# Performance work log

Measured on AMD Instinct MI355X. Metric: run time of the kernel, lower is better.

## Reference

```python
import jax, jax.numpy as jnp
import numpy as np
import math

B, N, DIM = 4, 2048, 768
HEADS, DIM_HEAD = 12, 64
SCALE = math.sqrt(DIM_HEAD)


def setup_inputs() -> dict:
    key = jax.random.key(0)
    ks = jax.random.split(key, 5)
    inner = HEADS * DIM_HEAD
    x = jax.random.normal(ks[0], (B, N, DIM), dtype=jnp.float32)
    # Linear weights stored as [in, out] so y = x @ W (equivalent to torch Linear with W.T)
    w_q = jax.random.normal(ks[1], (DIM, inner), dtype=jnp.float32) * 0.02
    w_k = jax.random.normal(ks[2], (DIM, inner), dtype=jnp.float32) * 0.02
    w_v = jax.random.normal(ks[3], (DIM, inner), dtype=jnp.float32) * 0.02
    w_o = jax.random.normal(ks[4], (inner, DIM), dtype=jnp.float32) * 0.02
    b_o = jnp.zeros((DIM,), dtype=jnp.float32)
    return {"x": x, "w_q": w_q, "w_k": w_k, "w_v": w_v, "w_o": w_o, "b_o": b_o}


def _split_heads(t):
    # [b, n, h*d] -> [b, h, n, d]
    b, n, _ = t.shape
    return t.reshape(b, n, HEADS, DIM_HEAD).transpose(0, 2, 1, 3)


def reference(x, w_q, w_k, w_v, w_o, b_o):
    # context = x (self-attention, kv_include_self=False)
    q = _split_heads(x @ w_q)  # [b,h,n,d]
    k = _split_heads(x @ w_k)
    v = _split_heads(x @ w_v)
    scores = jnp.einsum("bhnd,bhmd->bhnm", q, k) / SCALE  # [b,h,n,n]
    attn = jax.nn.softmax(scores, axis=-1)  # dropout p=0 -> identity
    h = jnp.einsum("bhnm,bhmd->bhnd", attn, v)  # [b,h,n,d]
    H = h.transpose(0, 2, 1, 3).reshape(x.shape[0], x.shape[1], HEADS * DIM_HEAD)
    out = H @ w_o + b_o
    return out
```

## Files before the change

### kernel.cpp

```cpp
#include <hip/hip_runtime.h>
#include <hip/hip_bf16.h>
#include <cstdint>
#include <cstddef>

#define HEADS 12
#define DHEAD 64
#define SEQ   2048
#define DIMM  768
#define BATCH 4
#define MROWS (BATCH*SEQ)
#define BH    (BATCH*HEADS)
#define SCL_Q 0.18033688011112042f

typedef __attribute__((ext_vector_type(8))) short short8;
typedef __attribute__((ext_vector_type(4))) short short4v;
typedef __attribute__((ext_vector_type(4))) float floatx4;

__device__ __forceinline__ unsigned short f2bf(float f) {
    union { float f; uint32_t u; } v; v.f = f;
    uint32_t u = v.u;
    u += 0x7fffu + ((u >> 16) & 1u);
    return (unsigned short)(u >> 16);
}
__device__ __forceinline__ float bf2f(unsigned short h) {
    union { uint32_t u; float f; } v; v.u = ((uint32_t)h) << 16;
    return v.f;
}
#if __has_builtin(__builtin_amdgcn_perm)
__device__ __forceinline__ uint32_t pkbf(float a, float b) {
    union { float f; uint32_t u; } ua, ub; ua.f = a; ub.f = b;
    return __builtin_amdgcn_perm(ub.u + 0x8000u, ua.u + 0x8000u, 0x07060302u);
}
#else
__device__ __forceinline__ uint32_t pkbf(float a, float b) {
    __hip_bfloat162 h = __float22bfloat162_rn(make_float2(a, b));
    uint32_t u; __builtin_memcpy(&u, &h, 4); return u;
}
#endif
__device__ __forceinline__ float fexp2(float x) {
#if __has_builtin(__builtin_amdgcn_exp2f)
    return __builtin_amdgcn_exp2f(x);
#else
    return exp2f(x);
#endif
}

#if __has_builtin(__builtin_amdgcn_global_load_lds)
#define HAVE_GLDS 1
__device__ __forceinline__ void glds16(const unsigned short* g, unsigned short* l) {
    __builtin_amdgcn_global_load_lds(
        (const __attribute__((address_space(1))) unsigned int*)g,
        (__attribute__((address_space(3))) unsigned int*)l, 16, 0, 0);
}
#else
#define HAVE_GLDS 0
#endif

__device__ __forceinline__ int detect_f32(const uint32_t* xw, int tid) {
    __shared__ int cnt_;
    if (tid == 0) cnt_ = 0;
    __syncthreads();
    uint32_t w = xw[(size_t)(tid & 255) * 4096];
    float av = fabsf(bf2f((unsigned short)(w & 0xFFFFu)));
    atomicAdd(&cnt_, (av >= 9.0949e-13f && av <= 256.0f) ? 1 : 0);
    __syncthreads();
    return (cnt_ < 192) ? 1 : 0;
}

__global__ __launch_bounds__(256) void prep(
    const void* __restrict__ x,
    const void* __restrict__ wq, const void* __restrict__ wk,
    const void* __restrict__ wv, const void* __restrict__ wo,
    unsigned short* __restrict__ xc,
    unsigned short* __restrict__ wtq, unsigned short* __restrict__ wtk,
    unsigned short* __restrict__ wtv, unsigned short* __restrict__ wto)
{
    const int tid = threadIdx.x;
    const int isf32 = detect_f32((const uint32_t*)x, tid);
    const int blk = blockIdx.x;

    if (blk < 2304) {
        __shared__ unsigned short tile[32][33];
        const int m = blk / 576, rr = blk % 576;
        const void* src; unsigned short* dst;
        switch (m) {
            case 0: src = wq; dst = wtq; break;
            case 1: src = wk; dst = wtk; break;
            case 2: src = wv; dst = wtv; break;
            default: src = wo; dst = wto; break;
        }
        const float* srcf = (const float*)src;
        const unsigned short* srcs = (const unsigned short*)src;
        const int tx = tid & 31, ty = tid >> 5;
        const int k0 = (rr % 24) * 32;
        const int n0 = (rr / 24) * 32;
        #pragma unroll
        for (int it = 0; it < 4; it++) {
            int r = ty + it * 8;
            size_t idx = (size_t)(k0 + r) * DIMM + n0 + tx;
            tile[r][tx] = isf32 ? f2bf(srcf[idx]) : srcs[idx];
        }
        __syncthreads();
        #pragma unroll
        for (int it = 0; it < 4; it++) {
            int r = ty + it * 8;
            dst[(size_t)(n0 + r) * DIMM + k0 + tx] = tile[tx][r];
        }
    } else {
        const size_t i0 = ((size_t)(blk - 2304) * 256 + tid) * 8;
        if (isf32) {
            const float* xf = (const float*)x;
            float4 a = *(const float4*)&xf[i0];
            float4 b = *(const float4*)&xf[i0 + 4];
            short8 s = { (short)f2bf(a.x), (short)f2bf(a.y), (short)f2bf(a.z), (short)f2bf(a.w),
                         (short)f2bf(b.x), (short)f2bf(b.y), (short)f2bf(b.z), (short)f2bf(b.w) };
            *(short8*)&xc[i0] = s;
        } else {
            *(short8*)&xc[i0] = *(const short8*)&((const unsigned short*)x)[i0];
        }
    }
}

__global__ __launch_bounds__(256) void gemm_bt(
    const unsigned short* __restrict__ A,
    const unsigned short* __restrict__ Wt0,
    const unsigned short* __restrict__ Wt1,
    const unsigned short* __restrict__ Wt2,
    void* __restrict__ O0, void* __restrict__ O1, void* __restrict__ O2,
    const void* __restrict__ bias,
    const uint32_t* __restrict__ xsample,
    int mode_base)
{
    const int mode = mode_base + blockIdx.z;
    const unsigned short* Wt = (mode == 1) ? Wt1 : (mode == 2) ? Wt2 : Wt0;
    void* OutV               = (mode == 1) ? O1  : (mode == 2) ? O2  : O0;
    unsigned short* Out16 = (unsigned short*)OutV;
    float* Outf           = (float*)OutV;

    int isf32 = 0;
    if (mode == 3) isf32 = detect_f32(xsample, threadIdx.x);

    __shared__ unsigned short As[128 * 64];
    __shared__ unsigned short Bs[128 * 64];

    const int tid  = threadIdx.x;
    const int wid  = tid >> 6;
    const int lane = tid & 63;
    const int l16  = lane & 15;
    const int quad = lane >> 4;
    const int wm   = wid & 1;
    const int wn   = wid >> 1;
    const int bm   = blockIdx.x * 128;
    const int bn   = blockIdx.y * 128;
    const bool swap = (mode != 2);

    floatx4 acc[4][4];
    #pragma unroll
    for (int i = 0; i < 4; i++)
        #pragma unroll
        for (int j = 0; j < 4; j++)
            acc[i][j] = floatx4{0.f, 0.f, 0.f, 0.f};

    for (int kk = 0; kk < DIMM; kk += 64) {
        #pragma unroll
        for (int t = 0; t < 4; t++) {
            const int c  = t * 256 + tid;
            const int r  = c >> 3;
            const int lc = (((c & 7) ^ (r & 7))) * 8;
#if HAVE_GLDS
            glds16(&A [(size_t)(bm + r) * DIMM + kk + lc], &As[(t * 256 + wid * 64) * 8]);
            glds16(&Wt[(size_t)(bn + r) * DIMM + kk + lc], &Bs[(t * 256 + wid * 64) * 8]);
#else
            *(short8*)&As[c * 8] = *(const short8*)&A [(size_t)(bm + r) * DIMM + kk + lc];
            *(short8*)&Bs[c * 8] = *(const short8*)&Wt[(size_t)(bn + r) * DIMM + kk + lc];
#endif
        }
        __syncthreads();
        #pragma unroll
        for (int ks = 0; ks < 2; ks++) {
            const int ph = ((ks * 4 + quad) ^ (l16 & 7)) * 8;
            short8 xa[4], wb[4];
            #pragma unroll
            for (int t = 0; t < 4; t++)
                xa[t] = *(const short8*)&As[(wm * 64 + t * 16 + l16) * 64 + ph];
            #pragma unroll
            for (int t = 0; t < 4; t++)
                wb[t] = *(const short8*)&Bs[(wn * 64 + t * 16 + l16) * 64 + ph];
            if (swap) {
                #pragma unroll
                for (int mt = 0; mt < 4; mt++)
                    #pragma unroll
                    for (int nt = 0; nt < 4; nt++)
                        acc[mt][nt] = __builtin_amdgcn_mfma_f32_16x16x32_bf16(
                            wb[mt], xa[nt], acc[mt][nt], 0, 0, 0);
            } else {
                #pragma unroll
                for (int mt = 0; mt < 4; mt++)
                    #pragma unroll
                    for (int nt = 0; nt < 4; nt++)
                        acc[mt][nt] = __builtin_amdgcn_mfma_f32_16x16x32_bf16(
                            xa[mt], wb[nt], acc[mt][nt], 0, 0, 0);
            }
        }
        __syncthreads();
    }

    if (!swap) {
        #pragma unroll
        for (int nt = 0; nt < 4; nt++) {
            const int gcol = bn + wn * 64 + nt * 16 + l16;
            #pragma unroll
            for (int mt = 0; mt < 4; mt++) {
                const int grow0 = bm + wm * 64 + mt * 16 + quad * 4;
                const int b = grow0 >> 11, n0 = grow0 & 2047;
                const int h = gcol >> 6,  d  = gcol & 63;
                size_t addr = ((size_t)(b * HEADS + h) * DHEAD + d) * SEQ + n0;
                short4v pk = { (short)f2bf(acc[mt][nt][0]), (short)f2bf(acc[mt][nt][1]),
                               (short)f2bf(acc[mt][nt][2]), (short)f2bf(acc[mt][nt][3]) };
                *(short4v*)&Out16[addr] = pk;
            }
        }
    } else {
        #pragma unroll
        for (int nt = 0; nt < 4; nt++) {
            const int grow = bm + wm * 64 + nt * 16 + l16;
            #pragma unroll
            for (int mt = 0; mt < 4; mt++) {
                const int gcol0 = bn + wn * 64 + mt * 16 + quad * 4;
                float v0 = acc[mt][nt][0], v1 = acc[mt][nt][1];
                float v2 = acc[mt][nt][2], v3 = acc[mt][nt][3];
                if (mode == 0) { v0 *= SCL_Q; v1 *= SCL_Q; v2 *= SCL_Q; v3 *= SCL_Q; }
                if (mode == 3) {
                    if (isf32) {
                        float4 bv = *(const float4*)&((const float*)bias)[gcol0];
                        float4 o = { v0 + bv.x, v1 + bv.y, v2 + bv.z, v3 + bv.w };
                        *(float4*)&Outf[(size_t)grow * DIMM + gcol0] = o;
                    } else {
                        const unsigned short* bb = &((const unsigned short*)bias)[gcol0];
                        short4v pk = { (short)f2bf(v0 + bf2f(bb[0])),
                                       (short)f2bf(v1 + bf2f(bb[1])),
                                       (short)f2bf(v2 + bf2f(bb[2])),
                                       (short)f2bf(v3 + bf2f(bb[3])) };
                        *(short4v*)&Out16[(size_t)grow * DIMM + gcol0] = pk;
                    }
                } else {
                    const int b = grow >> 11, n = grow & 2047;
                    const int h = gcol0 >> 6, d = gcol0 & 63;
                    size_t addr = ((size_t)(b * HEADS + h) * SEQ + n) * DHEAD + d;
                    short4v pk = { (short)f2bf(v0), (short)f2bf(v1),
                                   (short)f2bf(v2), (short)f2bf(v3) };
                    *(short4v*)&Out16[addr] = pk;
                }
            }
        }
    }
}

__global__ __launch_bounds__(256) void gemm_o64(
    const unsigned short* __restrict__ A,
    const unsigned short* __restrict__ Wt,
    void* __restrict__ Out,
    const void* __restrict__ bias,
    const uint32_t* __restrict__ xsample)
{
    unsigned short* Out16 = (unsigned short*)Out;
    float* Outf           = (float*)Out;
    const int isf32 = detect_f32(xsample, threadIdx.x);

    __shared__ unsigned short As[128 * 64];
    __shared__ unsigned short Bs[64 * 64];

    const int tid  = threadIdx.x;
    const int wid  = tid >> 6;
    const int lane = tid & 63;
    const int l16  = lane & 15;
    const int quad = lane >> 4;
    const int wm   = wid & 1;
    const int wn   = wid >> 1;
    const int bm   = blockIdx.x * 128;
    const int bn   = blockIdx.y * 64;

    floatx4 acc[2][4];
    #pragma unroll
    for (int i = 0; i < 2; i++)
        #pragma unroll
        for (int j = 0; j < 4; j++)
            acc[i][j] = floatx4{0.f, 0.f, 0.f, 0.f};

    for (int kk = 0; kk < DIMM; kk += 64) {
        #pragma unroll
        for (int t = 0; t < 4; t++) {
            const int c  = t * 256 + tid;
            const int r  = c >> 3;
            const int lc = (((c & 7) ^ (r & 7))) * 8;
#if HAVE_GLDS
            glds16(&A[(size_t)(bm + r) * DIMM + kk + lc], &As[(t * 256 + wid * 64) * 8]);
#else
            *(short8*)&As[c * 8] = *(const short8*)&A[(size_t)(bm + r) * DIMM + kk + lc];
#endif
        }
        #pragma unroll
        for (int t = 0; t < 2; t++) {
            const int c  = t * 256 + tid;
            const int r  = c >> 3;
            const int lc = (((c & 7) ^ (r & 7))) * 8;
#if HAVE_GLDS
            glds16(&Wt[(size_t)(bn + r) * DIMM + kk + lc], &Bs[(t * 256 + wid * 64) * 8]);
#else
            *(short8*)&Bs[c * 8] = *(const short8*)&Wt[(size_t)(bn + r) * DIMM + kk + lc];
#endif
        }
        __syncthreads();
        #pragma unroll
        for (int ks = 0; ks < 2; ks++) {
            const int ph = ((ks * 4 + quad) ^ (l16 & 7)) * 8;
            short8 xa[4], wb[2];
            #pragma unroll
            for (int t = 0; t < 4; t++)
                xa[t] = *(const short8*)&As[(wm * 64 + t * 16 + l16) * 64 + ph];
            #pragma unroll
            for (int t = 0; t < 2; t++)
                wb[t] = *(const short8*)&Bs[(wn * 32 + t * 16 + l16) * 64 + ph];
            #pragma unroll
            for (int mt = 0; mt < 2; mt++)
                #pragma unroll
                for (int nt = 0; nt < 4; nt++)
                    acc[mt][nt] = __builtin_amdgcn_mfma_f32_16x16x32_bf16(
                        wb[mt], xa[nt], acc[mt][nt], 0, 0, 0);
        }
        __syncthreads();
    }

    #pragma unroll
    for (int nt = 0; nt < 4; nt++) {
        const int grow = bm + wm * 64 + nt * 16 + l16;
        #pragma unroll
        for (int mt = 0; mt < 2; mt++) {
            const int gcol0 = bn + wn * 32 + mt * 16 + quad * 4;
            const float v0 = acc[mt][nt][0], v1 = acc[mt][nt][1];
            const float v2 = acc[mt][nt][2], v3 = acc[mt][nt][3];
            if (isf32) {
                float4 bv = *(const float4*)&((const float*)bias)[gcol0];
                float4 o = { v0 + bv.x, v1 + bv.y, v2 + bv.z, v3 + bv.w };
                *(float4*)&Outf[(size_t)grow * DIMM + gcol0] = o;
            } else {
                const unsigned short* bb = &((const unsigned short*)bias)[gcol0];
                short4v pk = { (short)f2bf(v0 + bf2f(bb[0])),
                               (short)f2bf(v1 + bf2f(bb[1])),
                               (short)f2bf(v2 + bf2f(bb[2])),
                               (short)f2bf(v3 + bf2f(bb[3])) };
                *(short4v*)&Out16[(size_t)grow * DIMM + gcol0] = pk;
            }
        }
    }
}

__global__ __launch_bounds__(256, 3) void attn(
    const unsigned short* __restrict__ Q,
    const unsigned short* __restrict__ K,
    const unsigned short* __restrict__ Vt,
    unsigned short* __restrict__ Hout)
{
    __shared__ unsigned short KsB[2 * 64 * 64];
    __shared__ unsigned short VsB[2 * 64 * 64];
    __shared__ unsigned short Ps[8][16 * 64];

    const int tid  = threadIdx.x;
    const int wid  = tid >> 6;
    const int lane = tid & 63;
    const int l16  = lane & 15;
    const int quad = lane >> 4;
    const int sw   = l16 & 7;

    const int bh = blockIdx.x % BH;
    const int qt = blockIdx.x / BH;

    short8 qf[2][2];
    #pragma unroll
    for (int t = 0; t < 2; t++) {
        const int qrow = qt * 128 + wid * 32 + t * 16 + l16;
        const size_t qbase = ((size_t)bh * SEQ + qrow) * DHEAD;
        qf[t][0] = *(const short8*)&Q[qbase + quad * 8];
        qf[t][1] = *(const short8*)&Q[qbase + 32 + quad * 8];
    }

    const short8 ones = { (short)0x3F80, (short)0x3F80, (short)0x3F80, (short)0x3F80,
                          (short)0x3F80, (short)0x3F80, (short)0x3F80, (short)0x3F80 };

    floatx4 ot[2][4];
    floatx4 acc_l[2];
    #pragma unroll
    for (int t = 0; t < 2; t++) {
        acc_l[t] = floatx4{0.f, 0.f, 0.f, 0.f};
        #pragma unroll
        for (int i = 0; i < 4; i++) ot[t][i] = floatx4{0.f, 0.f, 0.f, 0.f};
    }

    const size_t kbase = (size_t)bh * SEQ * DHEAD;
    const size_t vbase = (size_t)bh * DHEAD * SEQ;

    short8 rk[2], rv[2];
    #pragma unroll
    for (int j = 0; j < 2; j++) {
        const int c = tid + j * 256, r = c >> 3, c8 = (c & 7) * 8;
        const int g = ((c & 7) ^ (r & 7)) * 8;
        short8 tk = *(const short8*)&K[kbase + (size_t)r * DHEAD + c8];
        short8 tv = *(const short8*)&Vt[vbase + (size_t)r * SEQ + c8];
        *(short8*)&KsB[r * 64 + g] = tk;
        *(short8*)&VsB[r * 64 + g] = tv;
        rk[j] = *(const short8*)&K[kbase + (size_t)(64 + r) * DHEAD + c8];
        rv[j] = *(const short8*)&Vt[vbase + (size_t)r * SEQ + 64 + c8];
    }

    short8 vfr[2][4];
    short8 pfr[2][2];

    for (int kt = 0; kt < SEQ / 64; kt++) {
        const int cur = kt & 1;
        unsigned short* Kc = &KsB[cur * 4096];
        unsigned short* Kn = &KsB[(cur ^ 1) * 4096];
        unsigned short* Vn = &VsB[(cur ^ 1) * 4096];

        if (kt > 0) {
            #pragma unroll
            for (int ks = 0; ks < 2; ks++) {
                #pragma unroll
                for (int dt = 0; dt < 4; dt++)
                    vfr[ks][dt] = *(const short8*)
                        &Vn[(dt * 16 + l16) * 64 + ((ks * 4 + quad) ^ sw) * 8];
                #pragma unroll
                for (int t = 0; t < 2; t++)
                    pfr[ks][t] = *(const short8*)
                        &Ps[wid * 2 + t][l16 * 64 + ((ks * 4 + quad) ^ sw) * 8];
            }
        }
        __syncthreads();

        if (kt + 1 < SEQ / 64) {
            #pragma unroll
            for (int j = 0; j < 2; j++) {
                const int c = tid + j * 256, r = c >> 3;
                const int g = ((c & 7) ^ (r & 7)) * 8;
                *(short8*)&Kn[r * 64 + g] = rk[j];
                *(short8*)&Vn[r * 64 + g] = rv[j];
            }
        }
        if (kt + 2 < SEQ / 64) {
            #pragma unroll
            for (int j = 0; j < 2; j++) {
                const int c = tid + j * 256, r = c >> 3, c8 = (c & 7) * 8;
                rk[j] = *(const short8*)&K[kbase + (size_t)((kt + 2) * 64 + r) * DHEAD + c8];
                rv[j] = *(const short8*)&Vt[vbase + (size_t)r * SEQ + (kt + 2) * 64 + c8];
            }
        }

        uint2 pk[2][4];
        #pragma unroll
        for (int mt = 0; mt < 4; mt++) {
            const int krow = (mt * 16 + l16) * 64;
            short8 kf0 = *(const short8*)&Kc[krow + (quad ^ sw) * 8];
            short8 kf1 = *(const short8*)&Kc[krow + ((4 + quad) ^ sw) * 8];
            #pragma unroll
            for (int t = 0; t < 2; t++) {
                floatx4 a = floatx4{0.f, 0.f, 0.f, 0.f};
                a = __builtin_amdgcn_mfma_f32_16x16x32_bf16(kf0, qf[t][0], a, 0, 0, 0);
                a = __builtin_amdgcn_mfma_f32_16x16x32_bf16(kf1, qf[t][1], a, 0, 0, 0);
                pk[t][mt] = (uint2){ pkbf(fexp2(a[0]), fexp2(a[1])),
                                     pkbf(fexp2(a[2]), fexp2(a[3])) };
            }
        }

        if (kt > 0) {
            __builtin_amdgcn_s_setprio(1);
            #pragma unroll
            for (int ks = 0; ks < 2; ks++) {
                #pragma unroll
                for (int t = 0; t < 2; t++) {
                    #pragma unroll
                    for (int dt = 0; dt < 4; dt++)
                        ot[t][dt] = __builtin_amdgcn_mfma_f32_16x16x32_bf16(
                            vfr[ks][dt], pfr[ks][t], ot[t][dt], 0, 0, 0);
                    acc_l[t] = __builtin_amdgcn_mfma_f32_16x16x32_bf16(
                        ones, pfr[ks][t], acc_l[t], 0, 0, 0);
                }
            }
            __builtin_amdgcn_s_setprio(0);
        }

        #pragma unroll
        for (int t = 0; t < 2; t++)
            #pragma unroll
            for (int mt = 0; mt < 4; mt++)
                *(uint2*)&Ps[wid * 2 + t]
                    [l16 * 64 + ((2 * mt + (quad >> 1)) ^ sw) * 8 + (quad & 1) * 4]
                    = pk[t][mt];
    }

    {
        unsigned short* Vl = &VsB[((SEQ / 64 - 1) & 1) * 4096];
        #pragma unroll
        for (int ks = 0; ks < 2; ks++) {
            #pragma unroll
            for (int dt = 0; dt < 4; dt++)
                vfr[ks][dt] = *(const short8*)
                    &Vl[(dt * 16 + l16) * 64 + ((ks * 4 + quad) ^ sw) * 8];
            #pragma unroll
            for (int t = 0; t < 2; t++)
                pfr[ks][t] = *(const short8*)
                    &Ps[wid * 2 + t][l16 * 64 + ((ks * 4 + quad) ^ sw) * 8];
        }
        __builtin_amdgcn_s_setprio(1);
        #pragma unroll
        for (int ks = 0; ks < 2; ks++)
            #pragma unroll
            for (int t = 0; t < 2; t++) {
                #pragma unroll
                for (int dt = 0; dt < 4; dt++)
                    ot[t][dt] = __builtin_amdgcn_mfma_f32_16x16x32_bf16(
                        vfr[ks][dt], pfr[ks][t], ot[t][dt], 0, 0, 0);
                acc_l[t] = __builtin_amdgcn_mfma_f32_16x16x32_bf16(
                    ones, pfr[ks][t], acc_l[t], 0, 0, 0);
            }
        __builtin_amdgcn_s_setprio(0);
    }

    const int b = bh / HEADS, h = bh % HEADS;
    #pragma unroll
    for (int t = 0; t < 2; t++) {
        const float inv_l = 1.0f / acc_l[t][0];
        unsigned short* Pw = Ps[wid * 2 + t];
        #pragma unroll
        for (int dt = 0; dt < 4; dt++) {
            uint2 pk2 = { pkbf(ot[t][dt][0] * inv_l, ot[t][dt][1] * inv_l),
                          pkbf(ot[t][dt][2] * inv_l, ot[t][dt][3] * inv_l) };
            *(uint2*)&Pw[l16 * 64 + ((2 * dt + (quad >> 1)) ^ sw) * 8 + (quad & 1) * 4]
                = pk2;
        }
        const int q_r   = lane >> 2;
        const int dpart = (lane & 3) * 16;
        const int rsw   = q_r & 7;
        short8 h0 = *(const short8*)&Pw[q_r * 64 + ((2 * (lane & 3)) ^ rsw) * 8];
        short8 h1 = *(const short8*)&Pw[q_r * 64 + ((2 * (lane & 3) + 1) ^ rsw) * 8];
        const int growg = b * SEQ + qt * 128 + wid * 32 + t * 16 + q_r;
        const size_t oaddr = (size_t)growg * DIMM + h * DHEAD + dpart;
        *(short8*)&Hout[oaddr] = h0;
        *(short8*)&Hout[oaddr + 8] = h1;
    }
}

extern "C" void kernel_launch(void* const* d_in, const int* in_sizes, int n_in,
                              void* d_out, int out_size, void* d_ws, size_t ws_size,
                              hipStream_t stream)
{
    (void)in_sizes; (void)n_in; (void)out_size;
    const void* x  = d_in[0];
    const void* wq = d_in[1];
    const void* wk = d_in[2];
    const void* wv = d_in[3];
    const void* wo = d_in[4];
    const void* bo = d_in[5];

    char* ws = (char*)d_ws;
    const size_t SZ_QKV = (size_t)MROWS * DIMM * sizeof(unsigned short);
    const size_t SZ_W   = (size_t)DIMM * DIMM * sizeof(unsigned short);
    const size_t need = 5 * SZ_QKV + 4 * SZ_W;
    if (ws_size < need) return;

    unsigned short* xc   = (unsigned short*)(ws);
    unsigned short* Qws  = (unsigned short*)(ws + 1 * SZ_QKV);
    unsigned short* Kws  = (unsigned short*)(ws + 2 * SZ_QKV);
    unsigned short* Vtws = (unsigned short*)(ws + 3 * SZ_QKV);
    unsigned short* Hws  = (unsigned short*)(ws + 4 * SZ_QKV);
    unsigned short* Wtq  = (unsigned short*)(ws + 5 * SZ_QKV);
    unsigned short* Wtk  = (unsigned short*)(ws + 5 * SZ_QKV + SZ_W);
    unsigned short* Wtv  = (unsigned short*)(ws + 5 * SZ_QKV + 2 * SZ_W);
    unsigned short* Wto  = (unsigned short*)(ws + 5 * SZ_QKV + 3 * SZ_W);

    hipLaunchKernelGGL(prep, dim3(2304 + MROWS * DIMM / 2048), dim3(256), 0, stream,
                       x, wq, wk, wv, wo, xc, Wtq, Wtk, Wtv, Wto);
    hipLaunchKernelGGL(gemm_bt, dim3(64, 6, 3), dim3(256), 0, stream,
                       xc, Wtq, Wtk, Wtv, (void*)Qws, (void*)Kws, (void*)Vtws,
                       bo, (const uint32_t*)x, 0);
    hipLaunchKernelGGL(attn, dim3(BH * (SEQ / 128)), dim3(256), 0, stream,
                       Qws, Kws, Vtws, Hws);
    hipLaunchKernelGGL(gemm_o64, dim3(64, 12), dim3(256), 0, stream,
                       Hws, Wto, d_out, bo, (const uint32_t*)x);
}
```

Baseline: 233.5 us.

## Keep P in registers and feed PV with 16x16x16 MFMA instead of LDS round-trip

The exponentiated score tile P is no longer written to and read back from a per-wave LDS buffer. Because the QK^T MFMA output layout matches the 16x16x16 bf16 B-operand layout, P is passed straight from registers to the PV matmul, with V fragments loaded as 4-element chunks. This removes the Ps LDS traffic and 16 KB of shared memory, and the epilogue reuses the K buffer after a barrier. The cost is twice as many MFMA instructions, each half as wide, plus more register pressure from the V fragments.

Result: no change. 234.0 us (+0.2%).

```diff
diff --git a/kernel.cpp b/kernel.cpp
--- a/kernel.cpp
+++ b/kernel.cpp
@@ -42,6 +42,18 @@
     return __builtin_amdgcn_exp2f(x);
 #else
     return exp2f(x);
+#endif
+}
+
+__device__ __forceinline__ floatx4 mfma16(short4v a, short4v b, floatx4 c) {
+#if __has_builtin(__builtin_amdgcn_mfma_f32_16x16x16_bf16)
+    return __builtin_amdgcn_mfma_f32_16x16x16_bf16(a, b, c, 0, 0, 0);
+#elif __has_builtin(__builtin_amdgcn_mfma_f32_16x16x16bf16_1k)
+    return __builtin_amdgcn_mfma_f32_16x16x16bf16_1k(a, b, c, 0, 0, 0);
+#else
+    short8 a8 = { a[0], a[1], a[2], a[3], 0, 0, 0, 0 };
+    short8 b8 = { b[0], b[1], b[2], b[3], 0, 0, 0, 0 };
+    return __builtin_amdgcn_mfma_f32_16x16x32_bf16(a8, b8, c, 0, 0, 0);
 #endif
 }
 
@@ -363,7 +375,6 @@
 {
     __shared__ unsigned short KsB[2 * 64 * 64];
     __shared__ unsigned short VsB[2 * 64 * 64];
-    __shared__ unsigned short Ps[8][16 * 64];
 
     const int tid  = threadIdx.x;
     const int wid  = tid >> 6;
@@ -384,8 +395,7 @@
         qf[t][1] = *(const short8*)&Q[qbase + 32 + quad * 8];
     }
 
-    const short8 ones = { (short)0x3F80, (short)0x3F80, (short)0x3F80, (short)0x3F80,
-                          (short)0x3F80, (short)0x3F80, (short)0x3F80, (short)0x3F80 };
+    const short4v ones4 = { (short)0x3F80, (short)0x3F80, (short)0x3F80, (short)0x3F80 };
 
     floatx4 ot[2][4];
     floatx4 acc_l[2];
@@ -412,8 +422,8 @@
         rv[j] = *(const short8*)&Vt[vbase + (size_t)r * SEQ + 64 + c8];
     }
 
-    short8 vfr[2][4];
-    short8 pfr[2][2];
+    short4v vfr16[4][4];
+    short4v pkprev[2][4];
 
     for (int kt = 0; kt < SEQ / 64; kt++) {
         const int cur = kt & 1;
@@ -423,16 +433,12 @@
 
         if (kt > 0) {
             #pragma unroll
-            for (int ks = 0; ks < 2; ks++) {
+            for (int mt = 0; mt < 4; mt++)
                 #pragma unroll
                 for (int dt = 0; dt < 4; dt++)
-                    vfr[ks][dt] = *(const short8*)
-                        &Vn[(dt * 16 + l16) * 64 + ((ks * 4 + quad) ^ sw) * 8];
-                #pragma unroll
-                for (int t = 0; t < 2; t++)
-                    pfr[ks][t] = *(const short8*)
-                        &Ps[wid * 2 + t][l16 * 64 + ((ks * 4 + quad) ^ sw) * 8];
-            }
+                    vfr16[mt][dt] = *(const short4v*)
+                        &Vn[(dt * 16 + l16) * 64
+                            + ((2 * mt + (quad >> 1)) ^ sw) * 8 + (quad & 1) * 4];
         }
         __syncthreads();
 
@@ -473,15 +479,13 @@
         if (kt > 0) {
             __builtin_amdgcn_s_setprio(1);
             #pragma unroll
-            for (int ks = 0; ks < 2; ks++) {
+            for (int mt = 0; mt < 4; mt++) {
                 #pragma unroll
                 for (int t = 0; t < 2; t++) {
                     #pragma unroll
                     for (int dt = 0; dt < 4; dt++)
-                        ot[t][dt] = __builtin_amdgcn_mfma_f32_16x16x32_bf16(
-                            vfr[ks][dt], pfr[ks][t], ot[t][dt], 0, 0, 0);
-                    acc_l[t] = __builtin_amdgcn_mfma_f32_16x16x32_bf16(
-                        ones, pfr[ks][t], acc_l[t], 0, 0, 0);
+                        ot[t][dt] = mfma16(vfr16[mt][dt], pkprev[t][mt], ot[t][dt]);
+                    acc_l[t] = mfma16(ones4, pkprev[t][mt], acc_l[t]);
                 }
             }
             __builtin_amdgcn_s_setprio(0);
@@ -490,45 +494,41 @@
         #pragma unroll
         for (int t = 0; t < 2; t++)
             #pragma unroll
-            for (int mt = 0; mt < 4; mt++)
-                *(uint2*)&Ps[wid * 2 + t]
-                    [l16 * 64 + ((2 * mt + (quad >> 1)) ^ sw) * 8 + (quad & 1) * 4]
-                    = pk[t][mt];
+            for (int mt = 0; mt < 4; mt++) {
+                union { uint2 u; short4v s; } cv; cv.u = pk[t][mt];
+                pkprev[t][mt] = cv.s;
+            }
     }
 
     {
         unsigned short* Vl = &VsB[((SEQ / 64 - 1) & 1) * 4096];
         #pragma unroll
-        for (int ks = 0; ks < 2; ks++) {
+        for (int mt = 0; mt < 4; mt++)
             #pragma unroll
             for (int dt = 0; dt < 4; dt++)
-                vfr[ks][dt] = *(const short8*)
-                    &Vl[(dt * 16 + l16) * 64 + ((ks * 4 + quad) ^ sw) * 8];
-            #pragma unroll
-            for (int t = 0; t < 2; t++)
-                pfr[ks][t] = *(const short8*)
-                    &Ps[wid * 2 + t][l16 * 64 + ((ks * 4 + quad) ^ sw) * 8];
-        }
+                vfr16[mt][dt] = *(const short4v*)
+                    &Vl[(dt * 16 + l16) * 64
+                        + ((2 * mt + (quad >> 1)) ^ sw) * 8 + (quad & 1) * 4];
         __builtin_amdgcn_s_setprio(1);
         #pragma unroll
-        for (int ks = 0; ks < 2; ks++)
+        for (int mt = 0; mt < 4; mt++)
             #pragma unroll
             for (int t = 0; t < 2; t++) {
                 #pragma unroll
                 for (int dt = 0; dt < 4; dt++)
-                    ot[t][dt] = __builtin_amdgcn_mfma_f32_16x16x32_bf16(
-                        vfr[ks][dt], pfr[ks][t], ot[t][dt], 0, 0, 0);
-                acc_l[t] = __builtin_amdgcn_mfma_f32_16x16x32_bf16(
-                    ones, pfr[ks][t], acc_l[t], 0, 0, 0);
+                    ot[t][dt] = mfma16(vfr16[mt][dt], pkprev[t][mt], ot[t][dt]);
+                acc_l[t] = mfma16(ones4, pkprev[t][mt], acc_l[t]);
             }
         __builtin_amdgcn_s_setprio(0);
     }
+
+    __syncthreads();
 
     const int b = bh / HEADS, h = bh % HEADS;
     #pragma unroll
     for (int t = 0; t < 2; t++) {
         const float inv_l = 1.0f / acc_l[t][0];
-        unsigned short* Pw = Ps[wid * 2 + t];
+        unsigned short* Pw = &KsB[(wid * 2 + t) * 1024];
         #pragma unroll
         for (int dt = 0; dt < 4; dt++) {
             uint2 pk2 = { pkbf(ot[t][dt][0] * inv_l, ot[t][dt][1] * inv_l),
```
